# Kernel optimization log

Hardware: AMD Instinct MI355X
Metric: run time of the kernel (lower is better)

The kernel has to match this reference:

```python
import jax, jax.numpy as jnp
import numpy as np

B, L, S, V, I, H = 4096, 16, 512, 512, 512, 512  # batch, attn_length, attn_size, attn_vec_size, input_size, lstm hidden


def setup_inputs() -> dict:
    key = jax.random.key(0)
    ks = jax.random.split(key, 16)
    rn = lambda k, sh, sc=1.0: jax.random.normal(k, sh, dtype=jnp.float32) * sc
    return {
        "inputs": rn(ks[0], (B, I)),
        "cell_c": rn(ks[1], (B, H)),
        "cell_h": rn(ks[2], (B, H)),
        "attns": rn(ks[3], (B, S)),
        "attn_states": rn(ks[4], (B, L, S)),
        "W1": rn(ks[5], (I + S, I), 0.02),
        "b1": jnp.zeros((I,), jnp.float32),
        "Wx": rn(ks[6], (I, 4 * H), 0.02),
        "Wh": rn(ks[7], (H, 4 * H), 0.02),
        "b_lstm": jnp.zeros((4 * H,), jnp.float32),
        "W3": rn(ks[8], (2 * H, V), 0.02),
        "b3": jnp.zeros((V,), jnp.float32),
        "k": rn(ks[9], (1, 1, S, V), 0.02),
        "v": rn(ks[10], (1, 1, S, V), 0.02),
        "W2": rn(ks[11], (H + S, S), 0.02),
        "b2": jnp.zeros((S,), jnp.float32),
    }


def reference(inputs, cell_c, cell_h, attns, attn_states, W1, b1, Wx, Wh, b_lstm, W3, b3, k, v, W2, b2):
    # linear1: project [inputs; attns] -> cell input
    x = jnp.concatenate([inputs, attns], axis=1) @ W1 + b1  # [B, I]
    # LSTM cell step (gate order i, f, g, o)
    gates = x @ Wx + cell_h @ Wh + b_lstm  # [B, 4H]
    i, f, g, o = jnp.split(gates, 4, axis=1)
    c_new = jax.nn.sigmoid(f) * cell_c + jax.nn.sigmoid(i) * jnp.tanh(g)
    h_new = jax.nn.sigmoid(o) * jnp.tanh(c_new)
    # attention over attn_states with query = concat(new_state)
    query = jnp.concatenate([c_new, h_new], axis=1)  # [B, 2H]
    # 1x1 conv over [B, L, 1, S] with kernel [1,1,S,V] == matmul over S
    hf = jnp.einsum('bls,sv->blv', attn_states, k[0, 0])  # [B, L, V]
    y = query @ W3 + b3  # [B, V]
    t = jnp.tanh(hf + y[:, None, :])  # [B, L, V]
    # reduce_sum(v * t, [2,3]) with v [1,1,S,V] broadcast against t [B,L,1,V]
    # == einsum over V with v summed over its S axis (t independent of S axis)
    vsum = v[0, 0].sum(axis=0)  # [V]
    s = jnp.einsum('blv,v->bl', t, vsum)  # [B, L]
    a = jax.nn.softmax(s, axis=1)
    d = jnp.einsum('bl,bls->bs', a, attn_states)  # new_attns [B, S]
    # output projection on [cell_output; new_attns]
    output = jnp.concatenate([h_new, d], axis=1) @ W2 + b2  # [B, S]
    # shift attention window: drop oldest, append output
    new_attn_states = jnp.concatenate([attn_states[:, 1:, :], output[:, None, :]], axis=1)
    new_attn_states = new_attn_states.reshape(inputs.shape[0], L * S)
    return output, c_new, h_new, d, new_attn_states
```

## Files before the change

### kernel.cpp

```cpp
#include <hip/hip_runtime.h>
#include <hip/hip_bf16.h>
#include <math.h>

#define BB 4096
#define LL 16
#define SS 512
#define VV 512
#define II 512
#define HH 512

typedef __attribute__((ext_vector_type(4))) float f32x4;
typedef __attribute__((ext_vector_type(8))) short short8;

#define GLOBAL_AS __attribute__((address_space(1)))
#define LDS_AS __attribute__((address_space(3)))

__device__ __forceinline__ unsigned short f2bf(float f) {
    union { float f; unsigned u; } c; c.f = f;
    unsigned u = c.u + 0x7FFFu + ((c.u >> 16) & 1u);
    return (unsigned short)(u >> 16);
}
__device__ __forceinline__ float bf2f(unsigned short u) {
    union { unsigned u; float f; } c; c.u = ((unsigned)u) << 16;
    return c.f;
}
__device__ __forceinline__ float fast_tanh(float x) {
    return 1.f - 2.f / (__expf(2.f * x) + 1.f);
}

template<int MODE, int NF>
__global__ __launch_bounds__(256) void gemm_mfma(
    const ushort* __restrict__ A, const ushort* __restrict__ Bt,
    const float* __restrict__ bias, void* __restrict__ C, float* __restrict__ C2,
    int ldc, int M, int N, int K) {
    constexpr int BN = NF * 32;
    __shared__ ushort Als[128 * 64];
    __shared__ ushort Bls[BN * 64];
    const int tid  = threadIdx.x;
    const int lane = tid & 63;
    const int w    = tid >> 6;
    const int wm   = w >> 1, wn = w & 1;
    const int brow = blockIdx.y * 128;
    const int bcol = blockIdx.x * BN;
    f32x4 acc[4][NF] = {};
    const int nkt = K >> 6;
    for (int kt = 0; kt < nkt; ++kt) {
        __syncthreads();
        #pragma unroll
        for (int i = 0; i < 4; ++i) {
            int c0 = i * 256 + w * 64;
            int c  = c0 + lane;
            int row = c >> 3, sl = c & 7;
            const ushort* gp = A + (size_t)(brow + row) * K + kt * 64 + ((sl ^ (row & 7)) * 8);
            __builtin_amdgcn_global_load_lds((const GLOBAL_AS void*)gp,
                                             (LDS_AS void*)(Als + c0 * 8), 16, 0, 0);
        }
        #pragma unroll
        for (int i = 0; i < NF; ++i) {
            int c0 = i * 256 + w * 64;
            int c  = c0 + lane;
            int row = c >> 3, sl = c & 7;
            const ushort* gp = Bt + (size_t)(bcol + row) * K + kt * 64 + ((sl ^ (row & 7)) * 8);
            __builtin_amdgcn_global_load_lds((const GLOBAL_AS void*)gp,
                                             (LDS_AS void*)(Bls + c0 * 8), 16, 0, 0);
        }
        __syncthreads();
        const char* AlsB = (const char*)Als;
        const char* BlsB = (const char*)Bls;
        #pragma unroll
        for (int kh = 0; kh < 2; ++kh) {
            int ks = kh * 4 + (lane >> 4);
            short8 a[4], b[NF];
            #pragma unroll
            for (int m = 0; m < 4; ++m) {
                int row = wm * 64 + m * 16 + (lane & 15);
                a[m] = *(const short8*)(AlsB + (row * 8 + (ks ^ (row & 7))) * 16);
            }
            #pragma unroll
            for (int n = 0; n < NF; ++n) {
                int row = wn * (NF * 16) + n * 16 + (lane & 15);
                b[n] = *(const short8*)(BlsB + (row * 8 + (ks ^ (row & 7))) * 16);
            }
            #pragma unroll
            for (int m = 0; m < 4; ++m)
                #pragma unroll
                for (int n = 0; n < NF; ++n)
                    acc[m][n] = __builtin_amdgcn_mfma_f32_16x16x32_bf16(a[m], b[n], acc[m][n], 0, 0, 0);
        }
    }
    #pragma unroll
    for (int m = 0; m < 4; ++m)
        #pragma unroll
        for (int n = 0; n < NF; ++n)
            #pragma unroll
            for (int r = 0; r < 4; ++r) {
                int gm = brow + wm * 64 + m * 16 + (lane >> 4) * 4 + r;
                int gc = bcol + wn * (NF * 16) + n * 16 + (lane & 15);
                float v = acc[m][n][r] + bias[gc];
                if (MODE == 1) ((ushort*)C)[(size_t)gm * ldc + gc] = f2bf(v);
                else           ((float*)C)[(size_t)gm * ldc + gc] = v;
                if (MODE == 2) C2[((size_t)gm * 16 + 15) * 512 + gc] = v;
            }
}

__global__ __launch_bounds__(256) void gemm_gates(
    const ushort* __restrict__ A, const ushort* __restrict__ Bt,
    const float* __restrict__ bias, const float* __restrict__ cc,
    float* __restrict__ o_c, float* __restrict__ o_h,
    ushort* __restrict__ A4, ushort* __restrict__ A7) {
    __shared__ ushort Als[128 * 64];
    __shared__ ushort Bls[128 * 64];
    const int tid = threadIdx.x, lane = tid & 63, w = tid >> 6;
    const int l15 = lane & 15, l4 = lane >> 4;
    const int brow = blockIdx.y * 128;
    const int xb = blockIdx.x;
    f32x4 acc[2][8] = {};
    for (int kt = 0; kt < 16; ++kt) {
        __syncthreads();
        #pragma unroll
        for (int i = 0; i < 4; ++i) {
            int c0 = i * 256 + w * 64, c = c0 + lane;
            int row = c >> 3, sl = c & 7;
            const ushort* gp = A + (size_t)(brow + row) * 1024 + kt * 64 + ((sl ^ (row & 7)) * 8);
            __builtin_amdgcn_global_load_lds((const GLOBAL_AS void*)gp,
                                             (LDS_AS void*)(Als + c0 * 8), 16, 0, 0);
        }
        #pragma unroll
        for (int i = 0; i < 4; ++i) {
            int c0 = i * 256 + w * 64, c = c0 + lane;
            int row = c >> 3, sl = c & 7;
            const ushort* gp = Bt + (size_t)(xb * 128 + row) * 1024 + kt * 64 + ((sl ^ (row & 7)) * 8);
            __builtin_amdgcn_global_load_lds((const GLOBAL_AS void*)gp,
                                             (LDS_AS void*)(Bls + c0 * 8), 16, 0, 0);
        }
        __syncthreads();
        const char* AlsB = (const char*)Als;
        const char* BlsB = (const char*)Bls;
        #pragma unroll
        for (int kh = 0; kh < 2; ++kh) {
            int ks = kh * 4 + l4;
            short8 a[2], b[8];
            #pragma unroll
            for (int m = 0; m < 2; ++m) {
                int row = w * 32 + m * 16 + l15;
                a[m] = *(const short8*)(AlsB + (row * 8 + (ks ^ (row & 7))) * 16);
            }
            #pragma unroll
            for (int n = 0; n < 8; ++n) {
                int row = n * 16 + l15;
                b[n] = *(const short8*)(BlsB + (row * 8 + (ks ^ (row & 7))) * 16);
            }
            #pragma unroll
            for (int m = 0; m < 2; ++m)
                #pragma unroll
                for (int n = 0; n < 8; ++n)
                    acc[m][n] = __builtin_amdgcn_mfma_f32_16x16x32_bf16(a[m], b[n], acc[m][n], 0, 0, 0);
        }
    }
    #pragma unroll
    for (int ug = 0; ug < 2; ++ug) {
        const int h = (2 * xb + ug) * 16 + l15;
        #pragma unroll
        for (int m = 0; m < 2; ++m)
            #pragma unroll
            for (int r = 0; r < 4; ++r) {
                int gm = brow + w * 32 + m * 16 + l4 * 4 + r;
                float gi = acc[m][ug * 4 + 0][r] + bias[h];
                float gf = acc[m][ug * 4 + 1][r] + bias[512 + h];
                float gg = acc[m][ug * 4 + 2][r] + bias[1024 + h];
                float go = acc[m][ug * 4 + 3][r] + bias[1536 + h];
                float si = 1.f / (1.f + __expf(-gi));
                float sf = 1.f / (1.f + __expf(-gf));
                float so = 1.f / (1.f + __expf(-go));
                float cv = sf * cc[(size_t)gm * 512 + h] + si * tanhf(gg);
                float hn = so * tanhf(cv);
                o_c[(size_t)gm * 512 + h] = cv;
                o_h[(size_t)gm * 512 + h] = hn;
                A4[(size_t)gm * 1024 + h] = f2bf(cv);
                A4[(size_t)gm * 1024 + 512 + h] = f2bf(hn);
                A7[(size_t)gm * 1024 + h] = f2bf(hn);
            }
    }
}

__global__ __launch_bounds__(512, 4) void score_all(
    const float* __restrict__ ASf, const ushort* __restrict__ Bt,
    const float* __restrict__ Y, const float* __restrict__ vsum,
    float* __restrict__ o_ns, float* __restrict__ o_d, ushort* __restrict__ A7) {
    __shared__ ushort Als[64 * 64];
    __shared__ ushort Bls[512 * 64];
    __shared__ float sred[8][64];
    __shared__ float s_lds[64];
    const int tid  = threadIdx.x;
    const int lane = tid & 63;
    const int w    = tid >> 6;
    const int l15  = lane & 15, l4 = lane >> 4;
    const int brow = blockIdx.x * 64;
    const int bg0  = brow >> 4;
    f32x4 acc[4][4] = {};
    for (int kt = 0; kt < 8; ++kt) {
        __syncthreads();
        #pragma unroll
        for (int i = 0; i < 8; ++i) {
            int c0 = i * 512 + w * 64;
            int c  = c0 + lane;
            int row = c >> 3, sl = c & 7;
            const ushort* gp = Bt + (size_t)row * 512 + kt * 64 + ((sl ^ (row & 7)) * 8);
            __builtin_amdgcn_global_load_lds((const GLOBAL_AS void*)gp,
                                             (LDS_AS void*)(Bls + c0 * 8), 16, 0, 0);
        }
        {
            int chunk = tid;
            int row = chunk >> 3, slot = chunk & 7;
            int gslot = slot ^ (row & 7);
            const float* gp = ASf + (size_t)(brow + row) * 512 + kt * 64 + gslot * 8;
            float4 f0 = *(const float4*)gp;
            float4 f1 = *(const float4*)(gp + 4);
            if ((row & 15) != 0) {
                float* op = o_ns + (size_t)(brow + row - 1) * 512 + kt * 64 + gslot * 8;
                *(float4*)op = f0;
                *(float4*)(op + 4) = f1;
            }
            short8 pk;
            pk[0] = (short)f2bf(f0.x); pk[1] = (short)f2bf(f0.y);
            pk[2] = (short)f2bf(f0.z); pk[3] = (short)f2bf(f0.w);
            pk[4] = (short)f2bf(f1.x); pk[5] = (short)f2bf(f1.y);
            pk[6] = (short)f2bf(f1.z); pk[7] = (short)f2bf(f1.w);
            *(short8*)((char*)Als + chunk * 16) = pk;
        }
        __syncthreads();
        const char* AlsB = (const char*)Als;
        const char* BlsB = (const char*)Bls;
        #pragma unroll
        for (int kh = 0; kh < 2; ++kh) {
            int ks = kh * 4 + l4;
            short8 a[4], b[4];
            #pragma unroll
            for (int m = 0; m < 4; ++m) {
                int row = m * 16 + l15;
                a[m] = *(const short8*)(AlsB + (row * 8 + (ks ^ (row & 7))) * 16);
            }
            #pragma unroll
            for (int n = 0; n < 4; ++n) {
                int rowb = w * 64 + n * 16 + l15;
                b[n] = *(const short8*)(BlsB + (rowb * 8 + (ks ^ (rowb & 7))) * 16);
            }
            #pragma unroll
            for (int m = 0; m < 4; ++m)
                #pragma unroll
                for (int n = 0; n < 4; ++n)
                    acc[m][n] = __builtin_amdgcn_mfma_f32_16x16x32_bf16(a[m], b[n], acc[m][n], 0, 0, 0);
        }
    }
    float part[4][4] = {};
    #pragma unroll
    for (int m = 0; m < 4; ++m) {
        int yb = bg0 + m;
        #pragma unroll
        for (int n = 0; n < 4; ++n) {
            int gc = w * 64 + n * 16 + l15;
            float yv = Y[(size_t)yb * 512 + gc];
            float vs = vsum[gc];
            #pragma unroll
            for (int r = 0; r < 4; ++r)
                part[m][r] += fast_tanh(acc[m][n][r] + yv) * vs;
        }
    }
    #pragma unroll
    for (int m = 0; m < 4; ++m)
        #pragma unroll
        for (int r = 0; r < 4; ++r) {
            float v = part[m][r];
            v += __shfl_xor(v, 1); v += __shfl_xor(v, 2);
            v += __shfl_xor(v, 4); v += __shfl_xor(v, 8);
            if (l15 == 0) sred[w][m * 16 + l4 * 4 + r] = v;
        }
    __syncthreads();
    if (tid < 64) {
        float v = 0.f;
        #pragma unroll
        for (int q = 0; q < 8; ++q) v += sred[q][tid];
        s_lds[tid] = v;
    }
    __syncthreads();

    {
        const int bat = w >> 1;
        const int bg  = bg0 + bat;
        const int c   = (w & 1) * 256 + lane * 4;
        float mx = -1e30f;
        #pragma unroll
        for (int l = 0; l < LL; ++l) mx = fmaxf(mx, s_lds[bat * 16 + l]);
        float wgt[LL]; float sum = 0.f;
        #pragma unroll
        for (int l = 0; l < LL; ++l) { wgt[l] = __expf(s_lds[bat * 16 + l] - mx); sum += wgt[l]; }
        const float inv = 1.f / sum;
        float d0 = 0.f, d1 = 0.f, d2 = 0.f, d3 = 0.f;
        #pragma unroll
        for (int l = 0; l < LL; ++l) {
            float4 v = *(const float4*)(ASf + ((size_t)bg * 16 + l) * 512 + c);
            d0 += wgt[l] * v.x; d1 += wgt[l] * v.y;
            d2 += wgt[l] * v.z; d3 += wgt[l] * v.w;
        }
        d0 *= inv; d1 *= inv; d2 *= inv; d3 *= inv;
        float4 dv; dv.x = d0; dv.y = d1; dv.z = d2; dv.w = d3;
        *(float4*)(o_d + (size_t)bg * 512 + c) = dv;
        ushort4 uv; uv.x = f2bf(d0); uv.y = f2bf(d1); uv.z = f2bf(d2); uv.w = f2bf(d3);
        *(ushort4*)(A7 + (size_t)bg * 1024 + 512 + c) = uv;
    }
}

struct TrJob { const float* srcA; const float* srcB; int K0; ushort* dst; int N; int K; int perm; };
struct TrJobs { TrJob j[5]; };

__global__ void tr_cvt_all(TrJobs jobs) {
    TrJob jb = jobs.j[blockIdx.z];
    int bn = blockIdx.x, bk = blockIdx.y;
    if (bn * 32 >= jb.N || bk * 32 >= jb.K) return;
    __shared__ float tile[32][33];
    int tx = threadIdx.x, ty = threadIdx.y;
    #pragma unroll
    for (int j = 0; j < 4; ++j) {
        int k = bk * 32 + ty + j * 8;
        const float* s = (k < jb.K0) ? (jb.srcA + (size_t)k * jb.N)
                                     : (jb.srcB + (size_t)(k - jb.K0) * jb.N);
        tile[ty + j * 8][tx] = s[bn * 32 + tx];
    }
    __syncthreads();
    #pragma unroll
    for (int j = 0; j < 4; ++j) {
        int n = bn * 32 + ty + j * 8;
        int nd = n;
        if (jb.perm) {
            int g = n >> 9, u = n & 511;
            nd = (u >> 4) * 64 + g * 16 + (u & 15);
        }
        jb.dst[(size_t)nd * jb.K + bk * 32 + tx] = f2bf(tile[tx][ty + j * 8]);
    }
}

struct CvJobs { const float* src[3]; ushort* dst[3]; };
__global__ void cvt_all(CvJobs jobs) {
    const float* src = jobs.src[blockIdx.y];
    ushort* dst = jobs.dst[blockIdx.y];
    int idx = blockIdx.x * 256 + threadIdx.x;
    int i4 = idx & 127, row = idx >> 7;
    float4 v = *(const float4*)(src + (size_t)row * 512 + i4 * 4);
    ushort4 o; o.x = f2bf(v.x); o.y = f2bf(v.y); o.z = f2bf(v.z); o.w = f2bf(v.w);
    *(ushort4*)(dst + (size_t)row * 1024 + i4 * 4) = o;
}

__global__ void vsum_k(const float* __restrict__ Vm, float* __restrict__ out) {
    __shared__ float red[8][32];
    int tc = threadIdx.x & 31, ts = threadIdx.x >> 5;
    int v = blockIdx.x * 32 + tc;
    float acc = 0.f;
    for (int s = ts; s < SS; s += 8) acc += Vm[(size_t)s * VV + v];
    red[ts][tc] = acc;
    __syncthreads();
    if (ts == 0) {
        float t = 0.f;
        #pragma unroll
        for (int j = 0; j < 8; ++j) t += red[j][tc];
        out[v] = t;
    }
}

extern "C" void kernel_launch(void* const* d_in, const int* in_sizes, int n_in,
                              void* d_out, int out_size, void* d_ws, size_t ws_size,
                              hipStream_t stream) {
    const float* inputs      = (const float*)d_in[0];
    const float* cell_c      = (const float*)d_in[1];
    const float* cell_h      = (const float*)d_in[2];
    const float* attns       = (const float*)d_in[3];
    const float* attn_states = (const float*)d_in[4];
    const float* W1          = (const float*)d_in[5];
    const float* b1          = (const float*)d_in[6];
    const float* Wx          = (const float*)d_in[7];
    const float* Wh          = (const float*)d_in[8];
    const float* b_lstm      = (const float*)d_in[9];
    const float* W3          = (const float*)d_in[10];
    const float* b3          = (const float*)d_in[11];
    const float* kmat        = (const float*)d_in[12];
    const float* vmat        = (const float*)d_in[13];
    const float* W2          = (const float*)d_in[14];
    const float* b2          = (const float*)d_in[15];

    float* o_out = (float*)d_out;
    float* o_c   = o_out + (size_t)BB * HH;
    float* o_h   = o_c   + (size_t)BB * HH;
    float* o_d   = o_h   + (size_t)BB * HH;
    float* o_ns  = o_d   + (size_t)BB * SS;

    float* ws_y     = (float*)d_ws;
    float* ws_vsum  = ws_y + (size_t)BB * VV;
    ushort* A1    = (ushort*)(ws_vsum + VV);
    ushort* A2    = A1 + (size_t)BB * 1024;
    ushort* A4    = A2 + (size_t)BB * 1024;
    ushort* A7    = A4 + (size_t)BB * 1024;
    ushort* W1t   = A7 + (size_t)BB * 1024;
    ushort* WBt   = W1t + (size_t)512 * 1024;
    ushort* W3t   = WBt + (size_t)2048 * 1024;
    ushort* W2t   = W3t + (size_t)512 * 1024;
    ushort* kTt   = W2t + (size_t)512 * 1024;

    TrJobs tj;
    tj.j[0] = {W1, W1, 1024, W1t, 512, 1024, 0};
    tj.j[1] = {Wx, Wh, 512, WBt, 2048, 1024, 1};
    tj.j[2] = {W3, W3, 1024, W3t, 512, 1024, 0};
    tj.j[3] = {W2, W2, 1024, W2t, 512, 1024, 0};
    tj.j[4] = {kmat, kmat, 512, kTt, 512, 512, 0};
    tr_cvt_all<<<dim3(64, 32, 5), dim3(32, 8), 0, stream>>>(tj);
    CvJobs cj;
    cj.src[0] = inputs; cj.dst[0] = A1;
    cj.src[1] = attns;  cj.dst[1] = A1 + 512;
    cj.src[2] = cell_h; cj.dst[2] = A2 + 512;
    cvt_all<<<dim3(BB * 128 / 256, 3), 256, 0, stream>>>(cj);
    vsum_k<<<16, 256, 0, stream>>>(vmat, ws_vsum);

    gemm_mfma<1, 1><<<dim3(512 / 32, BB / 128), 256, 0, stream>>>(
        A1, W1t, b1, A2, nullptr, 1024, BB, 512, 1024);
    gemm_gates<<<dim3(16, BB / 128), 256, 0, stream>>>(
        A2, WBt, b_lstm, cell_c, o_c, o_h, A4, A7);
    gemm_mfma<0, 1><<<dim3(512 / 32, BB / 128), 256, 0, stream>>>(
        A4, W3t, b3, ws_y, nullptr, 512, BB, 512, 1024);
    score_all<<<BB * LL / 64, 512, 0, stream>>>(
        attn_states, kTt, ws_y, ws_vsum, o_ns, o_d, A7);
    gemm_mfma<2, 1><<<dim3(512 / 32, BB / 128), 256, 0, stream>>>(
        A7, W2t, b2, o_out, o_ns, 512, BB, 512, 1024);
}
```

Baseline: 237.5 us.

## Double-buffer score_all K-loop and move attn_states shift copy to softmax pass

```diff
diff --git a/kernel.cpp b/kernel.cpp
--- a/kernel.cpp
+++ b/kernel.cpp
@@ -187,8 +187,8 @@
     const float* __restrict__ ASf, const ushort* __restrict__ Bt,
     const float* __restrict__ Y, const float* __restrict__ vsum,
     float* __restrict__ o_ns, float* __restrict__ o_d, ushort* __restrict__ A7) {
-    __shared__ ushort Als[64 * 64];
-    __shared__ ushort Bls[512 * 64];
+    __shared__ ushort Als[2][64 * 32];
+    __shared__ ushort Bls[2][512 * 32];
     __shared__ float sred[8][64];
     __shared__ float s_lds[64];
     const int tid  = threadIdx.x;
@@ -198,52 +198,65 @@
     const int brow = blockIdx.x * 64;
     const int bg0  = brow >> 4;
     f32x4 acc[4][4] = {};
-    for (int kt = 0; kt < 8; ++kt) {
-        __syncthreads();
-        #pragma unroll
-        for (int i = 0; i < 8; ++i) {
-            int c0 = i * 512 + w * 64;
-            int c  = c0 + lane;
-            int row = c >> 3, sl = c & 7;
-            const ushort* gp = Bt + (size_t)row * 512 + kt * 64 + ((sl ^ (row & 7)) * 8);
+    float4 a0, a1;
+
+    auto stageB = [&](int kt, int buf) {
+        #pragma unroll
+        for (int i = 0; i < 4; ++i) {
+            int c = i * 512 + tid;
+            int row = c >> 2, sl = c & 3;
+            int ss = sl ^ ((row >> 1) & 3);
+            const ushort* gp = Bt + (size_t)row * 512 + kt * 32 + ss * 8;
             __builtin_amdgcn_global_load_lds((const GLOBAL_AS void*)gp,
-                                             (LDS_AS void*)(Bls + c0 * 8), 16, 0, 0);
+                (LDS_AS void*)((ushort*)&Bls[buf][0] + c * 8), 16, 0, 0);
+        }
+    };
+    auto loadA = [&](int kt) {
+        if (tid < 256) {
+            int row = tid >> 2, sl = tid & 3;
+            int ss = sl ^ ((row >> 1) & 3);
+            const float* gp = ASf + (size_t)(brow + row) * 512 + kt * 32 + ss * 8;
+            a0 = *(const float4*)gp;
+            a1 = *(const float4*)(gp + 4);
+        }
+    };
+    auto writeA = [&](int buf) {
+        if (tid < 256) {
+            short8 pk;
+            pk[0] = (short)f2bf(a0.x); pk[1] = (short)f2bf(a0.y);
+            pk[2] = (short)f2bf(a0.z); pk[3] = (short)f2bf(a0.w);
+            pk[4] = (short)f2bf(a1.x); pk[5] = (short)f2bf(a1.y);
+            pk[6] = (short)f2bf(a1.z); pk[7] = (short)f2bf(a1.w);
+            *(short8*)((char*)&Als[buf][0] + tid * 16) = pk;
+        }
+    };
+
+    stageB(0, 0);
+    loadA(0);
+    writeA(0);
+    __syncthreads();
+
+    for (int t = 0; t < 16; ++t) {
+        const int buf = t & 1;
+        if (t < 15) {
+            stageB(t + 1, buf ^ 1);
+            loadA(t + 1);
         }
         {
-            int chunk = tid;
-            int row = chunk >> 3, slot = chunk & 7;
-            int gslot = slot ^ (row & 7);
-            const float* gp = ASf + (size_t)(brow + row) * 512 + kt * 64 + gslot * 8;
-            float4 f0 = *(const float4*)gp;
-            float4 f1 = *(const float4*)(gp + 4);
-            if ((row & 15) != 0) {
-                float* op = o_ns + (size_t)(brow + row - 1) * 512 + kt * 64 + gslot * 8;
-                *(float4*)op = f0;
-                *(float4*)(op + 4) = f1;
-            }
-            short8 pk;
-            pk[0] = (short)f2bf(f0.x); pk[1] = (short)f2bf(f0.y);
-            pk[2] = (short)f2bf(f0.z); pk[3] = (short)f2bf(f0.w);
-            pk[4] = (short)f2bf(f1.x); pk[5] = (short)f2bf(f1.y);
-            pk[6] = (short)f2bf(f1.z); pk[7] = (short)f2bf(f1.w);
-            *(short8*)((char*)Als + chunk * 16) = pk;
-        }
-        __syncthreads();
-        const char* AlsB = (const char*)Als;
-        const char* BlsB = (const char*)Bls;
-        #pragma unroll
-        for (int kh = 0; kh < 2; ++kh) {
-            int ks = kh * 4 + l4;
+            const char* AlsB = (const char*)&Als[buf][0];
+            const char* BlsB = (const char*)&Bls[buf][0];
             short8 a[4], b[4];
             #pragma unroll
             for (int m = 0; m < 4; ++m) {
                 int row = m * 16 + l15;
-                a[m] = *(const short8*)(AlsB + (row * 8 + (ks ^ (row & 7))) * 16);
+                int ps = l4 ^ ((row >> 1) & 3);
+                a[m] = *(const short8*)(AlsB + row * 64 + ps * 16);
             }
             #pragma unroll
             for (int n = 0; n < 4; ++n) {
-                int rowb = w * 64 + n * 16 + l15;
-                b[n] = *(const short8*)(BlsB + (rowb * 8 + (ks ^ (rowb & 7))) * 16);
+                int row = w * 64 + n * 16 + l15;
+                int ps = l4 ^ ((row >> 1) & 3);
+                b[n] = *(const short8*)(BlsB + row * 64 + ps * 16);
             }
             #pragma unroll
             for (int m = 0; m < 4; ++m)
@@ -251,7 +264,10 @@
                 for (int n = 0; n < 4; ++n)
                     acc[m][n] = __builtin_amdgcn_mfma_f32_16x16x32_bf16(a[m], b[n], acc[m][n], 0, 0, 0);
         }
-    }
+        if (t < 15) writeA(buf ^ 1);
+        __syncthreads();
+    }
+
     float part[4][4] = {};
     #pragma unroll
     for (int m = 0; m < 4; ++m) {
@@ -299,6 +315,8 @@
         #pragma unroll
         for (int l = 0; l < LL; ++l) {
             float4 v = *(const float4*)(ASf + ((size_t)bg * 16 + l) * 512 + c);
+            if (l >= 1)
+                *(float4*)(o_ns + ((size_t)bg * 16 + l - 1) * 512 + c) = v;
             d0 += wgt[l] * v.x; d1 += wgt[l] * v.y;
             d2 += wgt[l] * v.z; d3 += wgt[l] * v.w;
         }
```

New measurement: 234.0 us. Within noise of the previous version (-1.4%).
